# Kernel optimization log

Hardware: AMD Instinct MI355X
Metric: run time of the kernel (lower is better)

The kernel has to match this reference:

```python
import jax, jax.numpy as jnp
import numpy as np

N_AGENTS = 512
HID = 256
OBS = 128


def setup_inputs() -> dict:
    key = jax.random.key(0)
    ks = jax.random.split(key, 10)
    s = 0.02  # weight init scale
    f32 = jnp.float32
    return {
        "inputs": jax.random.normal(ks[0], (N_AGENTS, OBS), f32),
        "fc1_w": jax.random.normal(ks[1], (HID, OBS), f32) * s,
        "fc1_b": jnp.zeros((HID,), f32),
        "in_proj_w": jax.random.normal(ks[2], (3 * HID, HID), f32) * s,
        "in_proj_b": jnp.zeros((3 * HID,), f32),
        "out_proj_w": jax.random.normal(ks[3], (HID, HID), f32) * s,
        "out_proj_b": jnp.zeros((HID,), f32),
        "fc2_w": jax.random.normal(ks[4], (HID, 2 * HID), f32) * s,
        "fc2_b": jnp.zeros((HID,), f32),
        "fc3_w": jax.random.normal(ks[5], (2, HID), f32) * s,
        "fc3_b": jnp.zeros((2,), f32),
        "vfc2_w": jax.random.normal(ks[6], (HID, HID * N_AGENTS), f32) * s,
        "vfc2_b": jnp.zeros((HID,), f32),
        "vfc3_w": jax.random.normal(ks[7], (1, HID), f32) * s,
        "vfc3_b": jnp.zeros((1,), f32),
    }


def reference(inputs, fc1_w, fc1_b, in_proj_w, in_proj_b, out_proj_w, out_proj_b,
              fc2_w, fc2_b, fc3_w, fc3_b, vfc2_w, vfc2_b, vfc3_w, vfc3_b):
    n = inputs.shape[0]
    d = fc1_w.shape[0]
    # per-agent embed
    hid = jax.nn.relu(inputs @ fc1_w.T + fc1_b)                 # [n, d]
    # single-head self-attention (torch MultiheadAttention, 1 head)
    qkv = hid @ in_proj_w.T + in_proj_b                         # [n, 3d]
    q, k, v = jnp.split(qkv, 3, axis=-1)
    scores = (q @ k.T) / jnp.sqrt(jnp.asarray(d, hid.dtype))    # [n, n]
    attn = jax.nn.softmax(scores, axis=-1)
    h = (attn @ v) @ out_proj_w.T + out_proj_b                  # [n, d]
    # all-pairs edge features restricted to strict upper triangle
    iu0, iu1 = jnp.triu_indices(n, 1)                           # P = n(n-1)/2
    pairs = jnp.concatenate([h[iu0], h[iu1]], axis=1)           # [P, 2d]
    x = jax.nn.relu(pairs @ fc2_w.T + fc2_b)                    # [P, d]
    action_out = jax.nn.softmax(x @ fc3_w.T + fc3_b, axis=-1)   # [P, 2]
    # value head over flattened node embeddings
    vh = jax.nn.relu(hid.reshape(1, -1) @ vfc2_w.T + vfc2_b)    # [1, d]
    value = vh @ vfc3_w.T + vfc3_b                              # [1, 1]
    value = jnp.broadcast_to(value, (action_out.shape[0], 1))   # [P, 1]
    return jnp.concatenate([action_out, value], axis=1)         # [P, 3]
```

## Files before the change

### kernel.cpp

```cpp
#include <hip/hip_runtime.h>
#include <math.h>

#define N_AG   512
#define HIDD   256
#define OBSD   128

__device__ __forceinline__ void fma4(float4& acc, float4 a, float4 b){
    acc.x += a.x*b.x; acc.y += a.y*b.y; acc.z += a.z*b.z; acc.w += a.w*b.w;
}
__device__ __forceinline__ float hsum(float4 a){ return (a.x+a.y)+(a.z+a.w); }

__global__ __launch_bounds__(256) void k_fc1(const float* __restrict__ in,
        const float* __restrict__ w, const float* __restrict__ b,
        float* __restrict__ hid){
    __shared__ float lin[8*OBSD];
    int at = blockIdx.y, ot = blockIdx.x, t = threadIdx.x;
    ((float4*)lin)[t] = ((const float4*)(in + at*8*OBSD))[t];
    __syncthreads();
    int ol = t & 63, g = t >> 6;
    int o = ot*64 + ol;
    const float4* w4 = (const float4*)(w + o*OBSD);
    const float4* la = (const float4*)(lin + (g*2)*OBSD);
    const float4* lb = (const float4*)(lin + (g*2+1)*OBSD);
    float4 a0 = {0,0,0,0}, a1 = {0,0,0,0};
    #pragma unroll
    for (int c = 0; c < OBSD/4; ++c){
        float4 wv = w4[c];
        fma4(a0, la[c], wv);
        fma4(a1, lb[c], wv);
    }
    float bb = b[o];
    int ag = at*8 + g*2;
    hid[ag*HIDD + o]     = fmaxf(hsum(a0) + bb, 0.f);
    hid[(ag+1)*HIDD + o] = fmaxf(hsum(a1) + bb, 0.f);
}

__global__ __launch_bounds__(256) void k_qkv(const float* __restrict__ hid,
        const float* __restrict__ w, const float* __restrict__ b,
        float* __restrict__ qkv){
    __shared__ float lin[8*HIDD];
    int at = blockIdx.y, ot = blockIdx.x, t = threadIdx.x;
    const float4* in4 = (const float4*)(hid + at*8*HIDD);
    ((float4*)lin)[t]       = in4[t];
    ((float4*)lin)[t + 256] = in4[t + 256];
    __syncthreads();
    int ol = t & 63, g = t >> 6;
    int o = ot*64 + ol;
    const float4* w4 = (const float4*)(w + o*HIDD);
    const float4* la = (const float4*)(lin + (g*2)*HIDD);
    const float4* lb = (const float4*)(lin + (g*2+1)*HIDD);
    float4 a0 = {0,0,0,0}, a1 = {0,0,0,0};
    #pragma unroll 16
    for (int c = 0; c < HIDD/4; ++c){
        float4 wv = w4[c];
        fma4(a0, la[c], wv);
        fma4(a1, lb[c], wv);
    }
    float bb = b[o];
    int ag = at*8 + g*2;
    qkv[ag*768 + o]     = hsum(a0) + bb;
    qkv[(ag+1)*768 + o] = hsum(a1) + bb;
}

__global__ __launch_bounds__(256) void k_attn_vpart(const float* __restrict__ qkv,
        const float* __restrict__ ow, const float* __restrict__ ob,
        const float* __restrict__ hid, const float* __restrict__ vw,
        float* __restrict__ hout, float* __restrict__ partial){
    int t = threadIdx.x;
    if (blockIdx.x >= 256){
        int id = blockIdx.x - 256;
        int chunk = id & 7, o = id >> 3;
        const float4* h4 = (const float4*)hid;
        const float4* w4 = (const float4*)vw;
        long base  = (long)chunk*4096;
        long wbase = (long)o*32768 + base;
        float4 acc4 = {0,0,0,0};
        #pragma unroll 4
        for (int it = 0; it < 16; ++it)
            fma4(acc4, h4[base + it*256 + t], w4[wbase + it*256 + t]);
        float acc = hsum(acc4);
        for (int off = 32; off; off >>= 1) acc += __shfl_xor(acc, off);
        __shared__ float redv[4];
        int lane = t & 63, wid = t >> 6;
        if (lane == 0) redv[wid] = acc;
        __syncthreads();
        if (t == 0) partial[o*8 + chunk] = redv[0]+redv[1]+redv[2]+redv[3];
        return;
    }
    int r0 = blockIdx.x*2;
    __shared__ float q2[2*HIDD];
    __shared__ float sc[2*512];
    __shared__ float av[2*HIDD];
    __shared__ float red[16];
    if (t < 128){
        int r = t >> 6, c4 = t & 63;
        ((float4*)q2)[r*64 + c4] = ((const float4*)(qkv + (r0+r)*768))[c4];
    }
    __syncthreads();
    const float4* qa = (const float4*)q2;
    const float4* qb = (const float4*)(q2 + HIDD);
    #pragma unroll
    for (int jj = 0; jj < 2; ++jj){
        int j = t + jj*256;
        const float4* k4 = (const float4*)(qkv + j*768 + HIDD);
        float4 acc0 = {0,0,0,0}, acc1 = {0,0,0,0};
        #pragma unroll 16
        for (int c = 0; c < HIDD/4; ++c){
            float4 kv = k4[c];
            fma4(acc0, qa[c], kv);
            fma4(acc1, qb[c], kv);
        }
        sc[j]       = hsum(acc0) * 0.0625f;
        sc[512 + j] = hsum(acc1) * 0.0625f;
    }
    __syncthreads();
    int lane = t & 63, wid = t >> 6;
    float s00 = sc[t], s01 = sc[t+256], s10 = sc[512+t], s11 = sc[512+t+256];
    float m0 = fmaxf(s00, s01), m1 = fmaxf(s10, s11);
    for (int off = 32; off; off >>= 1){
        m0 = fmaxf(m0, __shfl_xor(m0, off));
        m1 = fmaxf(m1, __shfl_xor(m1, off));
    }
    if (lane == 0){ red[wid] = m0; red[4+wid] = m1; }
    __syncthreads();
    m0 = fmaxf(fmaxf(red[0],red[1]), fmaxf(red[2],red[3]));
    m1 = fmaxf(fmaxf(red[4],red[5]), fmaxf(red[6],red[7]));
    float e00 = expf(s00-m0), e01 = expf(s01-m0), e10 = expf(s10-m1), e11 = expf(s11-m1);
    float t0 = e00+e01, t1 = e10+e11;
    for (int off = 32; off; off >>= 1){ t0 += __shfl_xor(t0, off); t1 += __shfl_xor(t1, off); }
    if (lane == 0){ red[8+wid] = t0; red[12+wid] = t1; }
    __syncthreads();
    float inv0 = 1.f/(red[8]+red[9]+red[10]+red[11]);
    float inv1 = 1.f/(red[12]+red[13]+red[14]+red[15]);
    sc[t] = e00*inv0; sc[t+256] = e01*inv0;
    sc[512+t] = e10*inv1; sc[512+t+256] = e11*inv1;
    __syncthreads();
    {
        float acc0 = 0.f, acc1 = 0.f;
        #pragma unroll 8
        for (int j = 0; j < 512; ++j){
            float vv = qkv[j*768 + 512 + t];
            acc0 += sc[j]*vv;
            acc1 += sc[512+j]*vv;
        }
        av[t] = acc0; av[HIDD+t] = acc1;
    }
    __syncthreads();
    {
        const float4* w4 = (const float4*)(ow + t*HIDD);
        const float4* a4 = (const float4*)av;
        const float4* b4 = (const float4*)(av + HIDD);
        float4 h0 = {0,0,0,0}, h1 = {0,0,0,0};
        #pragma unroll 16
        for (int c = 0; c < HIDD/4; ++c){
            float4 wv = w4[c];
            fma4(h0, a4[c], wv);
            fma4(h1, b4[c], wv);
        }
        float bb = ob[t];
        hout[r0*HIDD + t]     = hsum(h0) + bb;
        hout[(r0+1)*HIDD + t] = hsum(h1) + bb;
    }
}

__global__ __launch_bounds__(256) void k_ab_value(const float* __restrict__ hin,
        const float* __restrict__ w2, const float* __restrict__ b2,
        const float* __restrict__ partial, const float* __restrict__ vb,
        const float* __restrict__ v3w, const float* __restrict__ v3b,
        float* __restrict__ A, float* __restrict__ B, float* __restrict__ value){
    int t = threadIdx.x;
    if (blockIdx.x == 512){
        float s = vb[t];
        #pragma unroll
        for (int c = 0; c < 8; ++c) s += partial[t*8 + c];
        s = fmaxf(s, 0.f) * v3w[t];
        for (int off = 32; off; off >>= 1) s += __shfl_xor(s, off);
        __shared__ float redv[4];
        int lane = t & 63, wid = t >> 6;
        if (lane == 0) redv[wid] = s;
        __syncthreads();
        if (t == 0) value[0] = redv[0]+redv[1]+redv[2]+redv[3] + v3b[0];
        return;
    }
    __shared__ float lin[8*HIDD];
    int id = blockIdx.x, at = id >> 3, ot = id & 7;
    const float4* in4 = (const float4*)(hin + at*8*HIDD);
    ((float4*)lin)[t]       = in4[t];
    ((float4*)lin)[t + 256] = in4[t + 256];
    __syncthreads();
    int ol = t & 63, g = t >> 6;
    int o2 = ot*64 + ol;
    bool isA = o2 < HIDD;
    int o = isA ? o2 : o2 - HIDD;
    const float4* w4 = (const float4*)(w2 + o*512 + (isA ? 0 : HIDD));
    const float4* la = (const float4*)(lin + (g*2)*HIDD);
    const float4* lb = (const float4*)(lin + (g*2+1)*HIDD);
    float4 acc0 = {0,0,0,0}, acc1 = {0,0,0,0};
    #pragma unroll 16
    for (int c = 0; c < HIDD/4; ++c){
        float4 wv = w4[c];
        fma4(acc0, la[c], wv);
        fma4(acc1, lb[c], wv);
    }
    int a0 = at*8 + g*2;
    float* dst = isA ? A : B;
    float bb = isA ? b2[o] : 0.f;
    dst[a0*HIDD + o]     = hsum(acc0) + bb;
    dst[(a0+1)*HIDD + o] = hsum(acc1) + bb;
}

__global__ __launch_bounds__(256) void k_pairs(const float* __restrict__ A,
        const float* __restrict__ B, const float* __restrict__ w3,
        const float* __restrict__ b3, const float* __restrict__ value,
        float* __restrict__ out){
    int ti = blockIdx.x, tj = blockIdx.y;
    if (tj < ti) return;
    __shared__ float la[16*260], lb[16*260], lw[256];
    int t = threadIdx.x;
    #pragma unroll
    for (int l = 0; l < 4; ++l){
        int idx = l*256 + t;
        int r = idx >> 6, c4 = idx & 63;
        ((float4*)la)[r*65 + c4] = ((const float4*)A)[(ti*16 + r)*64 + c4];
        ((float4*)lb)[r*65 + c4] = ((const float4*)B)[(tj*16 + r)*64 + c4];
    }
    lw[t] = w3[t] - w3[256 + t];
    __syncthreads();
    float val = value[0];
    float bd  = b3[0] - b3[1];
    int il = t >> 4, jl = t & 15;
    int i = ti*16 + il, j = tj*16 + jl;
    if (j > i){
        const float4* a4 = (const float4*)(la + il*260);
        const float4* b4 = (const float4*)(lb + jl*260);
        const float4* w4 = (const float4*)lw;
        float4 acc = {0,0,0,0};
        #pragma unroll 8
        for (int c = 0; c < 64; ++c){
            float4 aa = a4[c], bb = b4[c], wv = w4[c];
            acc.x += fmaxf(aa.x + bb.x, 0.f)*wv.x;
            acc.y += fmaxf(aa.y + bb.y, 0.f)*wv.y;
            acc.z += fmaxf(aa.z + bb.z, 0.f)*wv.z;
            acc.w += fmaxf(aa.w + bb.w, 0.f)*wv.w;
        }
        float z = hsum(acc) + bd;
        float o0 = 1.f/(1.f + expf(-z));
        int p = i*511 - (i*(i-1))/2 + (j - i - 1);
        out[3*p]   = o0;
        out[3*p+1] = 1.f - o0;
        out[3*p+2] = val;
    }
}

extern "C" void kernel_launch(void* const* d_in, const int* in_sizes, int n_in,
                              void* d_out, int out_size, void* d_ws, size_t ws_size,
                              hipStream_t stream){
    const float* inputs = (const float*)d_in[0];
    const float* fc1_w  = (const float*)d_in[1];
    const float* fc1_b  = (const float*)d_in[2];
    const float* inp_w  = (const float*)d_in[3];
    const float* inp_b  = (const float*)d_in[4];
    const float* outp_w = (const float*)d_in[5];
    const float* outp_b = (const float*)d_in[6];
    const float* fc2_w  = (const float*)d_in[7];
    const float* fc2_b  = (const float*)d_in[8];
    const float* fc3_w  = (const float*)d_in[9];
    const float* fc3_b  = (const float*)d_in[10];
    const float* vfc2_w = (const float*)d_in[11];
    const float* vfc2_b = (const float*)d_in[12];
    const float* vfc3_w = (const float*)d_in[13];
    const float* vfc3_b = (const float*)d_in[14];
    float* out = (float*)d_out;
    float* ws  = (float*)d_ws;
    float* hid     = ws;
    float* qkv     = ws + 131072;
    float* h       = ws + 524288;
    float* A       = ws + 655360;
    float* B       = ws + 786432;
    float* partial = ws + 917504;
    float* value   = ws + 919552;

    k_fc1       <<<dim3(4, 64),  256, 0, stream>>>(inputs, fc1_w, fc1_b, hid);
    k_qkv       <<<dim3(12, 64), 256, 0, stream>>>(hid, inp_w, inp_b, qkv);
    k_attn_vpart<<<dim3(2304),   256, 0, stream>>>(qkv, outp_w, outp_b, hid, vfc2_w, h, partial);
    k_ab_value  <<<dim3(513),    256, 0, stream>>>(h, fc2_w, fc2_b, partial, vfc2_b, vfc3_w, vfc3_b, A, B, value);
    k_pairs     <<<dim3(32, 32), 256, 0, stream>>>(A, B, fc3_w, fc3_b, value, out);
}
```

Baseline: 314.2 us.

## Process four query rows per attention block and add occupancy launch bounds

The attention blocks now handle four query rows instead of two, so each K and V load and each out_proj weight read is reused across twice as many rows, and there are half as many attention blocks. Softmax now runs one row per wavefront with shuffle reductions only, which removes the shared-memory reduction barriers. The value-head partial dot uses two accumulators to shorten the dependency chain, and launch_bounds(256,2) plus smaller unroll factors are added across kernels. The cost is more registers and shared memory per attention block and fewer blocks to spread across the GPU.

```diff
diff --git a/kernel.cpp b/kernel.cpp
--- a/kernel.cpp
+++ b/kernel.cpp
@@ -10,7 +10,7 @@
 }
 __device__ __forceinline__ float hsum(float4 a){ return (a.x+a.y)+(a.z+a.w); }
 
-__global__ __launch_bounds__(256) void k_fc1(const float* __restrict__ in,
+__global__ __launch_bounds__(256, 2) void k_fc1(const float* __restrict__ in,
         const float* __restrict__ w, const float* __restrict__ b,
         float* __restrict__ hid){
     __shared__ float lin[8*OBSD];
@@ -35,7 +35,7 @@
     hid[(ag+1)*HIDD + o] = fmaxf(hsum(a1) + bb, 0.f);
 }
 
-__global__ __launch_bounds__(256) void k_qkv(const float* __restrict__ hid,
+__global__ __launch_bounds__(256, 2) void k_qkv(const float* __restrict__ hid,
         const float* __restrict__ w, const float* __restrict__ b,
         float* __restrict__ qkv){
     __shared__ float lin[8*HIDD];
@@ -50,7 +50,7 @@
     const float4* la = (const float4*)(lin + (g*2)*HIDD);
     const float4* lb = (const float4*)(lin + (g*2+1)*HIDD);
     float4 a0 = {0,0,0,0}, a1 = {0,0,0,0};
-    #pragma unroll 16
+    #pragma unroll 8
     for (int c = 0; c < HIDD/4; ++c){
         float4 wv = w4[c];
         fma4(a0, la[c], wv);
@@ -62,23 +62,25 @@
     qkv[(ag+1)*768 + o] = hsum(a1) + bb;
 }
 
-__global__ __launch_bounds__(256) void k_attn_vpart(const float* __restrict__ qkv,
+__global__ __launch_bounds__(256, 2) void k_attn_vpart(const float* __restrict__ qkv,
         const float* __restrict__ ow, const float* __restrict__ ob,
         const float* __restrict__ hid, const float* __restrict__ vw,
         float* __restrict__ hout, float* __restrict__ partial){
     int t = threadIdx.x;
-    if (blockIdx.x >= 256){
-        int id = blockIdx.x - 256;
+    if (blockIdx.x >= 128){
+        int id = blockIdx.x - 128;
         int chunk = id & 7, o = id >> 3;
         const float4* h4 = (const float4*)hid;
         const float4* w4 = (const float4*)vw;
         long base  = (long)chunk*4096;
         long wbase = (long)o*32768 + base;
-        float4 acc4 = {0,0,0,0};
+        float4 aa = {0,0,0,0}, ab = {0,0,0,0};
         #pragma unroll 4
-        for (int it = 0; it < 16; ++it)
-            fma4(acc4, h4[base + it*256 + t], w4[wbase + it*256 + t]);
-        float acc = hsum(acc4);
+        for (int it = 0; it < 8; ++it){
+            fma4(aa, h4[base + it*256 + t],       w4[wbase + it*256 + t]);
+            fma4(ab, h4[base + (it+8)*256 + t],   w4[wbase + (it+8)*256 + t]);
+        }
+        float acc = hsum(aa) + hsum(ab);
         for (int off = 32; off; off >>= 1) acc += __shfl_xor(acc, off);
         __shared__ float redv[4];
         int lane = t & 63, wid = t >> 6;
@@ -87,83 +89,92 @@
         if (t == 0) partial[o*8 + chunk] = redv[0]+redv[1]+redv[2]+redv[3];
         return;
     }
-    int r0 = blockIdx.x*2;
-    __shared__ float q2[2*HIDD];
-    __shared__ float sc[2*512];
-    __shared__ float av[2*HIDD];
-    __shared__ float red[16];
-    if (t < 128){
+    int r0 = blockIdx.x*4;
+    __shared__ float qs[4*HIDD];
+    __shared__ float sc[4*512];
+    __shared__ float av[4*HIDD];
+    {
         int r = t >> 6, c4 = t & 63;
-        ((float4*)q2)[r*64 + c4] = ((const float4*)(qkv + (r0+r)*768))[c4];
-    }
-    __syncthreads();
-    const float4* qa = (const float4*)q2;
-    const float4* qb = (const float4*)(q2 + HIDD);
+        ((float4*)qs)[t] = ((const float4*)(qkv + (r0+r)*768))[c4];
+    }
+    __syncthreads();
+    const float4* q0 = (const float4*)qs;
+    const float4* q1 = (const float4*)(qs + HIDD);
+    const float4* q2 = (const float4*)(qs + 2*HIDD);
+    const float4* q3 = (const float4*)(qs + 3*HIDD);
     #pragma unroll
     for (int jj = 0; jj < 2; ++jj){
         int j = t + jj*256;
         const float4* k4 = (const float4*)(qkv + j*768 + HIDD);
-        float4 acc0 = {0,0,0,0}, acc1 = {0,0,0,0};
-        #pragma unroll 16
+        float4 a0 = {0,0,0,0}, a1 = {0,0,0,0}, a2 = {0,0,0,0}, a3 = {0,0,0,0};
+        #pragma unroll 8
         for (int c = 0; c < HIDD/4; ++c){
             float4 kv = k4[c];
-            fma4(acc0, qa[c], kv);
-            fma4(acc1, qb[c], kv);
-        }
-        sc[j]       = hsum(acc0) * 0.0625f;
-        sc[512 + j] = hsum(acc1) * 0.0625f;
-    }
-    __syncthreads();
-    int lane = t & 63, wid = t >> 6;
-    float s00 = sc[t], s01 = sc[t+256], s10 = sc[512+t], s11 = sc[512+t+256];
-    float m0 = fmaxf(s00, s01), m1 = fmaxf(s10, s11);
-    for (int off = 32; off; off >>= 1){
-        m0 = fmaxf(m0, __shfl_xor(m0, off));
-        m1 = fmaxf(m1, __shfl_xor(m1, off));
-    }
-    if (lane == 0){ red[wid] = m0; red[4+wid] = m1; }
-    __syncthreads();
-    m0 = fmaxf(fmaxf(red[0],red[1]), fmaxf(red[2],red[3]));
-    m1 = fmaxf(fmaxf(red[4],red[5]), fmaxf(red[6],red[7]));
-    float e00 = expf(s00-m0), e01 = expf(s01-m0), e10 = expf(s10-m1), e11 = expf(s11-m1);
-    float t0 = e00+e01, t1 = e10+e11;
-    for (int off = 32; off; off >>= 1){ t0 += __shfl_xor(t0, off); t1 += __shfl_xor(t1, off); }
-    if (lane == 0){ red[8+wid] = t0; red[12+wid] = t1; }
-    __syncthreads();
-    float inv0 = 1.f/(red[8]+red[9]+red[10]+red[11]);
-    float inv1 = 1.f/(red[12]+red[13]+red[14]+red[15]);
-    sc[t] = e00*inv0; sc[t+256] = e01*inv0;
-    sc[512+t] = e10*inv1; sc[512+t+256] = e11*inv1;
-    __syncthreads();
-    {
-        float acc0 = 0.f, acc1 = 0.f;
+            fma4(a0, q0[c], kv);
+            fma4(a1, q1[c], kv);
+            fma4(a2, q2[c], kv);
+            fma4(a3, q3[c], kv);
+        }
+        sc[j]        = hsum(a0) * 0.0625f;
+        sc[512 + j]  = hsum(a1) * 0.0625f;
+        sc[1024 + j] = hsum(a2) * 0.0625f;
+        sc[1536 + j] = hsum(a3) * 0.0625f;
+    }
+    __syncthreads();
+    {
+        int wv = t >> 6, ln = t & 63;
+        float* row = sc + wv*512;
+        float vals[8];
+        float m = -1e30f;
+        #pragma unroll
+        for (int k = 0; k < 8; ++k){ vals[k] = row[ln + k*64]; m = fmaxf(m, vals[k]); }
+        for (int off = 32; off; off >>= 1) m = fmaxf(m, __shfl_xor(m, off));
+        float s = 0.f;
+        #pragma unroll
+        for (int k = 0; k < 8; ++k){ vals[k] = expf(vals[k] - m); s += vals[k]; }
+        for (int off = 32; off; off >>= 1) s += __shfl_xor(s, off);
+        float inv = 1.f / s;
+        #pragma unroll
+        for (int k = 0; k < 8; ++k) row[ln + k*64] = vals[k]*inv;
+    }
+    __syncthreads();
+    {
+        float4 p = {0,0,0,0};
         #pragma unroll 8
         for (int j = 0; j < 512; ++j){
             float vv = qkv[j*768 + 512 + t];
-            acc0 += sc[j]*vv;
-            acc1 += sc[512+j]*vv;
-        }
-        av[t] = acc0; av[HIDD+t] = acc1;
+            p.x += sc[j]*vv;
+            p.y += sc[512+j]*vv;
+            p.z += sc[1024+j]*vv;
+            p.w += sc[1536+j]*vv;
+        }
+        av[t] = p.x; av[HIDD+t] = p.y; av[2*HIDD+t] = p.z; av[3*HIDD+t] = p.w;
     }
     __syncthreads();
     {
         const float4* w4 = (const float4*)(ow + t*HIDD);
-        const float4* a4 = (const float4*)av;
-        const float4* b4 = (const float4*)(av + HIDD);
-        float4 h0 = {0,0,0,0}, h1 = {0,0,0,0};
-        #pragma unroll 16
+        const float4* a0 = (const float4*)av;
+        const float4* a1 = (const float4*)(av + HIDD);
+        const float4* a2 = (const float4*)(av + 2*HIDD);
+        const float4* a3 = (const float4*)(av + 3*HIDD);
+        float4 h0 = {0,0,0,0}, h1 = {0,0,0,0}, h2 = {0,0,0,0}, h3 = {0,0,0,0};
+        #pragma unroll 8
         for (int c = 0; c < HIDD/4; ++c){
             float4 wv = w4[c];
-            fma4(h0, a4[c], wv);
-            fma4(h1, b4[c], wv);
+            fma4(h0, a0[c], wv);
+            fma4(h1, a1[c], wv);
+            fma4(h2, a2[c], wv);
+            fma4(h3, a3[c], wv);
         }
         float bb = ob[t];
-        hout[r0*HIDD + t]     = hsum(h0) + bb;
-        hout[(r0+1)*HIDD + t] = hsum(h1) + bb;
-    }
-}
-
-__global__ __launch_bounds__(256) void k_ab_value(const float* __restrict__ hin,
+        hout[r0*HIDD + t]       = hsum(h0) + bb;
+        hout[(r0+1)*HIDD + t]   = hsum(h1) + bb;
+        hout[(r0+2)*HIDD + t]   = hsum(h2) + bb;
+        hout[(r0+3)*HIDD + t]   = hsum(h3) + bb;
+    }
+}
+
+__global__ __launch_bounds__(256, 2) void k_ab_value(const float* __restrict__ hin,
         const float* __restrict__ w2, const float* __restrict__ b2,
         const float* __restrict__ partial, const float* __restrict__ vb,
         const float* __restrict__ v3w, const float* __restrict__ v3b,
@@ -196,7 +207,7 @@
     const float4* la = (const float4*)(lin + (g*2)*HIDD);
     const float4* lb = (const float4*)(lin + (g*2+1)*HIDD);
     float4 acc0 = {0,0,0,0}, acc1 = {0,0,0,0};
-    #pragma unroll 16
+    #pragma unroll 8
     for (int c = 0; c < HIDD/4; ++c){
         float4 wv = w4[c];
         fma4(acc0, la[c], wv);
@@ -209,7 +220,7 @@
     dst[(a0+1)*HIDD + o] = hsum(acc1) + bb;
 }
 
-__global__ __launch_bounds__(256) void k_pairs(const float* __restrict__ A,
+__global__ __launch_bounds__(256, 2) void k_pairs(const float* __restrict__ A,
         const float* __restrict__ B, const float* __restrict__ w3,
         const float* __restrict__ b3, const float* __restrict__ value,
         float* __restrict__ out){
@@ -282,7 +293,7 @@
 
     k_fc1       <<<dim3(4, 64),  256, 0, stream>>>(inputs, fc1_w, fc1_b, hid);
     k_qkv       <<<dim3(12, 64), 256, 0, stream>>>(hid, inp_w, inp_b, qkv);
-    k_attn_vpart<<<dim3(2304),   256, 0, stream>>>(qkv, outp_w, outp_b, hid, vfc2_w, h, partial);
+    k_attn_vpart<<<dim3(2176),   256, 0, stream>>>(qkv, outp_w, outp_b, hid, vfc2_w, h, partial);
     k_ab_value  <<<dim3(513),    256, 0, stream>>>(h, fc2_w, fc2_b, partial, vfc2_b, vfc3_w, vfc3_b, A, B, value);
     k_pairs     <<<dim3(32, 32), 256, 0, stream>>>(A, B, fc3_w, fc3_b, value, out);
 }
```

New measurement: 304.8 us. 1.03x faster.
